# Kernel optimization log

Measured on AMD Instinct MI355X. Metric: run time of the kernel, lower is better.

The kernel has to match this reference:

```python
import jax, jax.numpy as jnp
import numpy as np

D = 1024      # EMBEDDING_DIM
H = 16        # ATTENTION_HEADS
HD = 64       # HEAD_DIM
B, S = 4, 2048
EPS = 1e-5


def setup_inputs() -> dict:
    key = jax.random.key(0)
    ks = jax.random.split(key, 16)
    std = 0.02
    inp = {
        "x": jax.random.normal(ks[0], (B, S, D), dtype=jnp.float32),
        # per-head Q/K/V weights stacked: [H, D, HD]
        "Wq": jax.random.normal(ks[1], (H, D, HD), dtype=jnp.float32) * std,
        "Wk": jax.random.normal(ks[2], (H, D, HD), dtype=jnp.float32) * std,
        "Wv": jax.random.normal(ks[3], (H, D, HD), dtype=jnp.float32) * std,
        "bq": jnp.zeros((H, HD), dtype=jnp.float32),
        "bk": jnp.zeros((H, HD), dtype=jnp.float32),
        "bv": jnp.zeros((H, HD), dtype=jnp.float32),
        "Wo": jax.random.normal(ks[4], (D, D), dtype=jnp.float32) * std,
        "bo": jnp.zeros((D,), dtype=jnp.float32),
        "W1": jax.random.normal(ks[5], (D, 4 * D), dtype=jnp.float32) * std,
        "b1": jnp.zeros((4 * D,), dtype=jnp.float32),
        "W2": jax.random.normal(ks[6], (4 * D, D), dtype=jnp.float32) * std,
        "b2": jnp.zeros((D,), dtype=jnp.float32),
        # single shared LayerNorm (same module used for both pre-norms)
        "gamma": jnp.ones((D,), dtype=jnp.float32),
        "beta": jnp.zeros((D,), dtype=jnp.float32),
    }
    return inp


def _layer_norm(x, gamma, beta):
    mu = jnp.mean(x, axis=-1, keepdims=True)
    var = jnp.mean(jnp.square(x - mu), axis=-1, keepdims=True)
    return (x - mu) * jax.lax.rsqrt(var + EPS) * gamma + beta


def _block(x, Wq, Wk, Wv, bq, bk, bv, Wo, bo, W1, b1, W2, b2, gamma, beta):
    # pre-norm attention
    h = _layer_norm(x, gamma, beta)                     # [B,S,D]
    Q = jnp.einsum('bsd,hdk->bhsk', h, Wq) + bq[None, :, None, :]
    K = jnp.einsum('bsd,hdk->bhsk', h, Wk) + bk[None, :, None, :]
    V = jnp.einsum('bsd,hdk->bhsk', h, Wv) + bv[None, :, None, :]
    scores = jnp.einsum('bhsk,bhtk->bhst', Q, K) / jnp.sqrt(jnp.float32(HD))
    causal = jnp.tril(jnp.ones((S, S), dtype=bool))     # True = keep
    scores = jnp.where(causal[None, None], scores, -jnp.inf)
    attn = jax.nn.softmax(scores, axis=-1)              # [B,H,S,S]
    out = jnp.einsum('bhst,bhtk->bhsk', attn, V)        # [B,H,S,HD]
    out = out.transpose(0, 2, 1, 3).reshape(x.shape[0], x.shape[1], D)
    x = x + out @ Wo + bo
    # pre-norm MLP (shared layer norm params)
    h2 = _layer_norm(x, gamma, beta)
    mlp = jax.nn.gelu(h2 @ W1 + b1, approximate=False) @ W2 + b2
    return x + mlp


def reference(x, Wq, Wk, Wv, bq, bk, bv, Wo, bo, W1, b1, W2, b2, gamma, beta):
    return _block(x, Wq, Wk, Wv, bq, bk, bv, Wo, bo, W1, b1, W2, b2, gamma, beta)
```

## Files before the change

kernel.cpp:

```cpp
#include <hip/hip_runtime.h>
#include <hip/hip_bf16.h>

typedef __bf16  bf16x8 __attribute__((ext_vector_type(8)));
typedef float   f32x4  __attribute__((ext_vector_type(4)));
typedef short   s16x8  __attribute__((ext_vector_type(8)));

typedef const __attribute__((address_space(1))) void g_void;
typedef __attribute__((address_space(3))) void l_void;

__device__ __forceinline__ short f2b(float x) {
    __hip_bfloat16 h = __float2bfloat16(x);
    return __builtin_bit_cast(short, h);
}

__device__ __forceinline__ int pk2(float lo, float hi) {
    return (int)(unsigned short)f2b(lo) | ((int)f2b(hi) << 16);
}

__device__ __forceinline__ float fast_gelu(float v) {
    const float a = fminf(2.3022082f * (v + 0.044715f * v * v * v), 126.0f);
    const float t = exp2f(a);
    return v * t / (t + 1.0f);
}

__device__ __forceinline__ f32x4 mfma16(s16x8 a, s16x8 b, f32x4 c) {
    return __builtin_amdgcn_mfma_f32_16x16x32_bf16(
        __builtin_bit_cast(bf16x8, a), __builtin_bit_cast(bf16x8, b), c, 0, 0, 0);
}

__global__ __launch_bounds__(256) void transpose_bf16(
    const float* __restrict__ src, short* __restrict__ dst, int R, int C) {
    __shared__ float tile[32][33];
    src += (size_t)blockIdx.z * R * C;
    dst += (size_t)blockIdx.z * R * C;
    const int c0 = blockIdx.x * 32, r0 = blockIdx.y * 32;
    const int tx = threadIdx.x & 31, ty = threadIdx.x >> 5;
#pragma unroll
    for (int i = 0; i < 32; i += 8)
        tile[ty + i][tx] = src[(size_t)(r0 + ty + i) * C + c0 + tx];
    __syncthreads();
#pragma unroll
    for (int i = 0; i < 32; i += 8)
        dst[(size_t)(c0 + ty + i) * R + r0 + tx] = f2b(tile[tx][ty + i]);
}

__global__ __launch_bounds__(256) void concat_bias(
    const float* __restrict__ bq, const float* __restrict__ bk,
    const float* __restrict__ bv, float* __restrict__ o) {
    int i = blockIdx.x * 256 + threadIdx.x;
    if (i < 1024)      o[i] = bq[i];
    else if (i < 2048) o[i] = bk[i - 1024];
    else if (i < 3072) o[i] = bv[i - 2048];
}

__global__ __launch_bounds__(256) void ln_bf16(
    const float* __restrict__ x, const float* __restrict__ gamma,
    const float* __restrict__ beta, short* __restrict__ out) {
    __shared__ float red[8];
    const int row = blockIdx.x, tid = threadIdx.x;
    const float4 v = *(const float4*)(x + (size_t)row * 1024 + tid * 4);
    float s = v.x + v.y + v.z + v.w;
    float q = v.x * v.x + v.y * v.y + v.z * v.z + v.w * v.w;
#pragma unroll
    for (int off = 32; off > 0; off >>= 1) {
        s += __shfl_xor(s, off);
        q += __shfl_xor(q, off);
    }
    if ((tid & 63) == 0) { red[(tid >> 6) * 2] = s; red[(tid >> 6) * 2 + 1] = q; }
    __syncthreads();
    s = red[0] + red[2] + red[4] + red[6];
    q = red[1] + red[3] + red[5] + red[7];
    const float mu = s * (1.0f / 1024.0f);
    const float var = q * (1.0f / 1024.0f) - mu * mu;
    const float rs = rsqrtf(var + 1e-5f);
    const float4 g  = *(const float4*)(gamma + tid * 4);
    const float4 bt = *(const float4*)(beta + tid * 4);
    short4 o;
    o.x = f2b((v.x - mu) * rs * g.x + bt.x);
    o.y = f2b((v.y - mu) * rs * g.y + bt.y);
    o.z = f2b((v.z - mu) * rs * g.z + bt.z);
    o.w = f2b((v.w - mu) * rs * g.w + bt.w);
    *(short4*)(out + (size_t)row * 1024 + tid * 4) = o;
}

template <int MODE, int SWZ>
__global__ __launch_bounds__(512) void gemm_bf16(
    const short* __restrict__ A, const short* __restrict__ Bt,
    const float* __restrict__ bias, const float* __restrict__ resid,
    float* __restrict__ outf, short* __restrict__ outb, short* __restrict__ vt,
    int M, int N, int K) {
    __shared__ __align__(16) short As[2 * 128 * 32];
    __shared__ __align__(16) short Bs[2 * 128 * 32];

    const int tid = threadIdx.x;
    const int wave = tid >> 6, lane = tid & 63;
    const int l16 = lane & 15, quad = lane >> 4;
    const int wm = wave & 3, wn = wave >> 2;
    const int gx = gridDim.x;
    const int g = blockIdx.y * gx + blockIdx.x;
    const int xcd = g & 7, s = g >> 3;
    int m0, n0;
    if (SWZ == 0) {
        const int nband = gx >> 3;
        const int sm = s / nband;
        const int sn = s - sm * nband;
        m0 = sm * 128;
        n0 = (xcd * nband + sn) * 128;
    } else {
        const int mband = gridDim.y >> 3;
        const int sm = s / gx;
        m0 = (xcd * mband + sm) * 128;
        n0 = (s - sm * gx) * 128;
    }
    const int lrow = lane >> 2;
    const int lcol = (lane & 3) * 8;

    f32x4 acc[2][4] = {};

    for (int kk = 0; kk < K; kk += 64) {
#pragma unroll
        for (int p = 0; p < 2; ++p) {
            const int r = wave * 16 + lrow;
            const short* ga = A + (size_t)(m0 + r) * K + kk + p * 32 + lcol;
            short* la = &As[p * 4096 + wave * 512];
            __builtin_amdgcn_global_load_lds((g_void*)ga, (l_void*)la, 16, 0, 0);
            const short* gb = Bt + (size_t)(n0 + r) * K + kk + p * 32 + lcol;
            short* lb = &Bs[p * 4096 + wave * 512];
            __builtin_amdgcn_global_load_lds((g_void*)gb, (l_void*)lb, 16, 0, 0);
        }
        __syncthreads();
#pragma unroll
        for (int p = 0; p < 2; ++p) {
            s16x8 a[2], b[4];
#pragma unroll
            for (int t = 0; t < 2; ++t)
                a[t] = *(const s16x8*)&As[p * 4096 + (wm * 32 + t * 16 + l16) * 32 + quad * 8];
#pragma unroll
            for (int t = 0; t < 4; ++t)
                b[t] = *(const s16x8*)&Bs[p * 4096 + (wn * 64 + t * 16 + l16) * 32 + quad * 8];
#pragma unroll
            for (int mt = 0; mt < 2; ++mt)
#pragma unroll
                for (int nt = 0; nt < 4; ++nt)
                    acc[mt][nt] = mfma16(a[mt], b[nt], acc[mt][nt]);
        }
        __syncthreads();
    }

#pragma unroll
    for (int mt = 0; mt < 2; ++mt) {
#pragma unroll
        for (int nt = 0; nt < 4; ++nt) {
            const int row = m0 + wm * 32 + mt * 16 + quad * 4;
            const int col = n0 + wn * 64 + nt * 16 + l16;
            const float bc = bias[col];
            float v[4];
#pragma unroll
            for (int r = 0; r < 4; ++r) v[r] = acc[mt][nt][r] + bc;

            if (MODE == 1) {
#pragma unroll
                for (int r = 0; r < 4; ++r) {
                    const size_t rr = (size_t)(row + r);
                    outf[rr * N + col] = v[r] + resid[rr * N + col];
                }
            } else {
#pragma unroll
                for (int r = 0; r < 4; ++r)
                    outb[(size_t)(row + r) * N + col] = f2b(fast_gelu(v[r]));
            }
        }
    }
}


#define MM(MH, NH, AF, BB)                                                   \
    _Pragma("unroll") for (int p = 0; p < 2; ++p)                            \
        _Pragma("unroll") for (int ii = 0; ii < 4; ++ii)                     \
            _Pragma("unroll") for (int jj = 0; jj < 2; ++jj)                 \
                acc[(MH) * 4 + ii][(NH) * 2 + jj] =                          \
                    mfma16(AF[ii][p], BB[jj][p],                             \
                           acc[(MH) * 4 + ii][(NH) * 2 + jj]);

#define PH_A                                                                 \
    __builtin_amdgcn_s_barrier();                                            \
    asm volatile("s_waitcnt lgkmcnt(0)" ::: "memory");                       \
    __builtin_amdgcn_sched_barrier(0);                                       \
    __builtin_amdgcn_s_setprio(1);

#define PH_B                                                                 \
    __builtin_amdgcn_s_setprio(0);                                           \
    __builtin_amdgcn_sched_barrier(0);

#define PH_C                                                                 \
    __builtin_amdgcn_sched_barrier(0);                                       \
    __builtin_amdgcn_s_barrier();                                            \
    __builtin_amdgcn_sched_barrier(0);

#define KTILE(BUF, S1, S2, S3, S4)                                           \
    {                                                                        \
        s16x8 af[4][2], bl[2][2], bh[2][2];                                  \
                                        \
        _Pragma("unroll") for (int ii = 0; ii < 4; ++ii)                     \
            _Pragma("unroll") for (int p = 0; p < 2; ++p)                    \
                af[ii][p] = LDA(BUF, ii, p);                                 \
        _Pragma("unroll") for (int jj = 0; jj < 2; ++jj)                     \
            _Pragma("unroll") for (int p = 0; p < 2; ++p)                    \
                bl[jj][p] = LDB(BUF, jj, p);                                 \
        asm volatile("s_waitcnt lgkmcnt(8)" ::: "memory");                   \
        PH_A;                                                                \
        MM(0, 0, af, bl);                                                    \
        PH_B;                                                                \
        S1;                                                                  \
        PH_C;                                                                \
                                         \
        _Pragma("unroll") for (int jj = 0; jj < 2; ++jj)                     \
            _Pragma("unroll") for (int p = 0; p < 2; ++p)                    \
                bh[jj][p] = LDB(BUF, 2 + jj, p);                             \
        PH_A;                                                                \
        MM(0, 1, af, bh);                                                    \
        PH_B;                                                                \
        S2;                                                                  \
        PH_C;                                                                \
                                         \
        _Pragma("unroll") for (int ii = 0; ii < 4; ++ii)                     \
            _Pragma("unroll") for (int p = 0; p < 2; ++p)                    \
                af[ii][p] = LDA(BUF, 4 + ii, p);                             \
        PH_A;                                                                \
        MM(1, 1, af, bh);                                                    \
        PH_B;                                                                \
        S3;                                                                  \
        PH_C;                                                                \
                          \
        PH_A;                                                                \
        MM(1, 0, af, bl);                                                    \
        PH_B;                                                                \
        S4;                                                                  \
        asm volatile("s_waitcnt vmcnt(6)" ::: "memory");                     \
        PH_C;                                                                \
    }

template <int MODE>
__global__ __launch_bounds__(512, 2) void gemm256(
    const short* __restrict__ A, const short* __restrict__ Bt,
    const float* __restrict__ bias, const float* __restrict__ resid,
    float* __restrict__ outf, short* __restrict__ outb, short* __restrict__ vt,
    int M, int N, int K) {
    __shared__ __align__(16) short As[32768];
    __shared__ __align__(16) short Bs[32768];

    const int tid = threadIdx.x;
    const int wave = tid >> 6, lane = tid & 63;
    const int l16 = lane & 15, quad = lane >> 4;
    const int wm = wave >> 2, wn = wave & 3;

    const int nwg = gridDim.x;
    const int g = blockIdx.x;
    const int wgid = (g & 7) * (nwg >> 3) + (g >> 3);
    const int mtiles = M >> 8;
    const int m0 = (wgid % mtiles) << 8;
    const int n0 = (wgid / mtiles) << 8;

    const int rc = l16 * 32 + ((quad * 8) ^ ((l16 >> 3) << 4));
    const int a_rd = wm * 8192 + rc;
    const int b_rd = (wn >> 1) * 8192 + (wn & 1) * 4096 + rc;

    auto LDA = [&](int buf, int i, int p) {
        return *(const s16x8*)&As[buf * 16384 + a_rd + (i * 2 + p) * 512];
    };
    auto LDB = [&](int buf, int j, int p) {
        return *(const s16x8*)&Bs[buf * 16384 + b_rd + (j * 2 + p) * 512];
    };

    int r0, c0, r1, c1;
    {
        int s = tid * 16;
        int lin = s ^ (((s >> 9) & 1) << 5);
        r0 = ((lin >> 11) << 4) + ((lin >> 6) & 15);
        c0 = (((lin >> 10) & 1) << 5) + ((lin & 63) >> 1);
        s = (tid + 512) * 16;
        lin = s ^ (((s >> 9) & 1) << 5);
        r1 = ((lin >> 11) << 4) + ((lin >> 6) & 15);
        c1 = (((lin >> 10) & 1) << 5) + ((lin & 63) >> 1);
    }

    const short* gA = A + (size_t)m0 * K;
    const short* gB = Bt + (size_t)n0 * K;

    auto STAGE = [&](const short* gbase, int half, int kk, short* lds) {
        const short* s0 = gbase + (size_t)(half * 128 + r0) * K + kk + c0;
        const short* s1 = gbase + (size_t)(half * 128 + r1) * K + kk + c1;
        short* d0 = lds + half * 8192 + wave * 512;
        short* d1 = lds + half * 8192 + 4096 + wave * 512;
        __builtin_amdgcn_global_load_lds((g_void*)s0, (l_void*)d0, 16, 0, 0);
        __builtin_amdgcn_global_load_lds((g_void*)s1, (l_void*)d1, 16, 0, 0);
    };

    f32x4 acc[8][4] = {};

    STAGE(gB, 0, 0, Bs);
    STAGE(gB, 1, 0, Bs);
    STAGE(gA, 0, 0, As);
    STAGE(gA, 1, 0, As);
    asm volatile("s_waitcnt vmcnt(4)" ::: "memory");
    STAGE(gB, 0, 64, Bs + 16384);
    STAGE(gB, 1, 64, Bs + 16384);
    STAGE(gA, 0, 64, As + 16384);
    asm volatile("s_waitcnt vmcnt(6)" ::: "memory");
    __builtin_amdgcn_s_barrier();
    __builtin_amdgcn_sched_barrier(0);

    const int NI = K >> 7;
    for (int it = 0; it < NI; ++it) {
        const int kT1 = (2 * it + 1) * 64;
        int kT2 = (2 * it + 2) * 64;
        if (kT2 > K - 64) kT2 = K - 64;
        int kT3 = (2 * it + 3) * 64;
        if (kT3 > K - 64) kT3 = K - 64;

        KTILE(0,
              STAGE(gA, 1, kT1, As + 16384),
              STAGE(gB, 0, kT2, Bs),
              STAGE(gB, 1, kT2, Bs),
              STAGE(gA, 0, kT2, As));
        KTILE(1,
              STAGE(gA, 1, kT2, As),
              STAGE(gB, 0, kT3, Bs + 16384),
              STAGE(gB, 1, kT3, Bs + 16384),
              STAGE(gA, 0, kT3, As + 16384));
    }
    asm volatile("s_waitcnt vmcnt(0)" ::: "memory");

#pragma unroll
    for (int i = 0; i < 8; ++i) {
#pragma unroll
        for (int j = 0; j < 4; ++j) {
            const int row = m0 + wm * 128 + i * 16 + quad * 4;
            const int col = n0 + wn * 64 + j * 16 + l16;
            const float bc = bias[col];
            float v[4];
#pragma unroll
            for (int r = 0; r < 4; ++r) v[r] = acc[i][j][r] + bc;

            if (MODE == 0) {
                const int sel = col >> 10, within = col & 1023;
                const int h = within >> 6, hd = within & 63;
                const size_t bidx = (size_t)row >> 11, sp = row & 2047;
                if (sel == 0) {
#pragma unroll
                    for (int r = 0; r < 4; ++r) v[r] *= 0.18033688011112042f;
                }
                if (sel < 2) {
#pragma unroll
                    for (int r = 0; r < 4; ++r)
                        outb[(size_t)sel * (8192ull * 1024) +
                             ((bidx * 16 + h) * 2048 + sp + r) * 64 + hd] = f2b(v[r]);
                } else {
                    short4 o4;
                    o4.x = f2b(v[0]); o4.y = f2b(v[1]);
                    o4.z = f2b(v[2]); o4.w = f2b(v[3]);
                    *(short4*)&vt[((bidx * 16 + h) * 64 + hd) * 2048 + sp] = o4;
                }
            } else if (MODE == 1) {
#pragma unroll
                for (int r = 0; r < 4; ++r) {
                    const size_t rr = (size_t)(row + r);
                    outf[rr * N + col] = v[r] + resid[rr * N + col];
                }
            } else {
#pragma unroll
                for (int r = 0; r < 4; ++r)
                    outb[(size_t)(row + r) * N + col] = f2b(fast_gelu(v[r]));
            }
        }
    }
}

#undef KTILE
#undef PH_A
#undef PH_B
#undef PH_C
#undef MM

__global__ __launch_bounds__(256) void attn_kernel(
    const short* __restrict__ Q, const short* __restrict__ K,
    const short* __restrict__ Vt, short* __restrict__ O) {
    const int bid = blockIdx.x;
    const int xcd = bid & 7;
    const int sub = (bid >> 3) & 7;
    const int grp = bid >> 6;
    const int bh  = grp * 8 + xcd;
    const int h = bh & 15, b = bh >> 4;
    const int gq = sub;
    const int tid = threadIdx.x, wave = tid >> 6, lane = tid & 63;
    const int l16 = lane & 15, quad = lane >> 4;

    __shared__ __align__(16) short Ks[2][64 * 72];
    __shared__ __align__(16) short Vts[2][64 * 72];
    __shared__ __align__(16) short Ps[4][16 * 72];

    const size_t bhoff = (size_t)bh * (2048ull * 64);
    const int srow = tid >> 2;
    const int sseg = (tid & 3) * 16;

    const int qts[4] = {gq, 15 - gq, 16 + gq, 31 - gq};

    for (int pass = 0; pass < 4; ++pass) {
        const int qt = qts[pass];
        const int q0 = qt * 64;
        const int q_lane = q0 + wave * 16 + l16;

        const short* qrow = Q + bhoff + (size_t)q_lane * 64;
        s16x8 bq0 = *(const s16x8*)(qrow + quad * 8);
        s16x8 bq1 = *(const s16x8*)(qrow + 32 + quad * 8);

        f32x4 oacc[4] = {};
        float lsum = 0.0f;

        s16x8 k0, k1, v0, v1;
        {
            const short* kg = K + bhoff + (size_t)srow * 64 + sseg;
            k0 = *(const s16x8*)kg;
            k1 = *(const s16x8*)(kg + 8);
            const short* vg = Vt + bhoff + (size_t)srow * 2048 + sseg;
            v0 = *(const s16x8*)vg;
            v1 = *(const s16x8*)(vg + 8);
        }

        for (int j = 0; j <= qt; ++j) {
            const int buf = j & 1;
            *(s16x8*)&Ks[buf][srow * 72 + sseg]      = k0;
            *(s16x8*)&Ks[buf][srow * 72 + sseg + 8]  = k1;
            *(s16x8*)&Vts[buf][srow * 72 + sseg]     = v0;
            *(s16x8*)&Vts[buf][srow * 72 + sseg + 8] = v1;
            __syncthreads();

            if (j < qt) {
                const short* kg = K + bhoff + (size_t)((j + 1) * 64 + srow) * 64 + sseg;
                k0 = *(const s16x8*)kg;
                k1 = *(const s16x8*)(kg + 8);
                const short* vg = Vt + bhoff + (size_t)srow * 2048 + (j + 1) * 64 + sseg;
                v0 = *(const s16x8*)vg;
                v1 = *(const s16x8*)(vg + 8);
            }

            f32x4 st[4];
#pragma unroll
            for (int s = 0; s < 4; ++s) {
                s16x8 ak0 = *(const s16x8*)&Ks[buf][(s * 16 + l16) * 72 + quad * 8];
                s16x8 ak1 = *(const s16x8*)&Ks[buf][(s * 16 + l16) * 72 + 32 + quad * 8];
                f32x4 c = {};
                c = mfma16(ak0, bq0, c);
                c = mfma16(ak1, bq1, c);
                st[s] = c;
            }
            if (j == qt) {
#pragma unroll
                for (int s = 0; s < 4; ++s)
#pragma unroll
                    for (int r = 0; r < 4; ++r) {
                        const int t = j * 64 + s * 16 + quad * 4 + r;
                        if (t > q_lane) st[s][r] = -3000.0f;
                    }
            }
            float rs = 0.0f;
#pragma unroll
            for (int s = 0; s < 4; ++s) {
#pragma unroll
                for (int r = 0; r < 4; ++r) {
                    st[s][r] = exp2f(st[s][r]);
                    rs += st[s][r];
                }
                int2 pw;
                pw.x = pk2(st[s][0], st[s][1]);
                pw.y = pk2(st[s][2], st[s][3]);
                *(int2*)&Ps[wave][l16 * 72 + s * 16 + quad * 4] = pw;
            }
            rs += __shfl_xor(rs, 16);
            rs += __shfl_xor(rs, 32);
            lsum += rs;

            asm volatile("s_waitcnt lgkmcnt(0)" ::: "memory");
            s16x8 ap0 = *(const s16x8*)&Ps[wave][l16 * 72 + quad * 8];
            s16x8 ap1 = *(const s16x8*)&Ps[wave][l16 * 72 + 32 + quad * 8];

#pragma unroll
            for (int nt = 0; nt < 4; ++nt) {
                s16x8 bv0 = *(const s16x8*)&Vts[buf][(nt * 16 + l16) * 72 + quad * 8];
                s16x8 bv1 = *(const s16x8*)&Vts[buf][(nt * 16 + l16) * 72 + 32 + quad * 8];
                oacc[nt] = mfma16(ap0, bv0, oacc[nt]);
                oacc[nt] = mfma16(ap1, bv1, oacc[nt]);
            }
        }
        __syncthreads();

        float inv[4];
#pragma unroll
        for (int r = 0; r < 4; ++r)
            inv[r] = 1.0f / __shfl(lsum, quad * 4 + r, 64);
#pragma unroll
        for (int nt = 0; nt < 4; ++nt)
#pragma unroll
            for (int r = 0; r < 4; ++r) {
                const int row = q0 + wave * 16 + quad * 4 + r;
                O[((size_t)b * 2048 + row) * 1024 + h * 64 + nt * 16 + l16] =
                    f2b(oacc[nt][r] * inv[r]);
            }
    }
}

extern "C" void kernel_launch(void* const* d_in, const int* in_sizes, int n_in,
                              void* d_out, int out_size, void* d_ws, size_t ws_size,
                              hipStream_t stream) {
    const float* x     = (const float*)d_in[0];
    const float* Wq    = (const float*)d_in[1];
    const float* Wk    = (const float*)d_in[2];
    const float* Wv    = (const float*)d_in[3];
    const float* bq    = (const float*)d_in[4];
    const float* bk    = (const float*)d_in[5];
    const float* bv    = (const float*)d_in[6];
    const float* Wo    = (const float*)d_in[7];
    const float* bo    = (const float*)d_in[8];
    const float* W1    = (const float*)d_in[9];
    const float* b1    = (const float*)d_in[10];
    const float* W2    = (const float*)d_in[11];
    const float* b2    = (const float*)d_in[12];
    const float* gamma = (const float*)d_in[13];
    const float* beta  = (const float*)d_in[14];
    float* out = (float*)d_out;

    char* ws = (char*)d_ws;
    size_t off = 0;
    auto alloc = [&](size_t bytes) -> char* {
        char* p = ws + off;
        off += (bytes + 255) & ~(size_t)255;
        return p;
    };
    short* h1    = (short*)alloc(8192ull * 1024 * 2);
    short* btqkv = (short*)alloc(3072ull * 1024 * 2);
    short* btwo  = (short*)alloc(1024ull * 1024 * 2);
    short* btw1  = (short*)alloc(4096ull * 1024 * 2);
    short* btw2  = (short*)alloc(1024ull * 4096 * 2);
    float* bqkv  = (float*)alloc(3072ull * 4);
    short* qkv   = (short*)alloc(2ull * 8192 * 1024 * 2);
    short* vt    = (short*)alloc(8192ull * 1024 * 2);
    short* aout  = (short*)alloc(8192ull * 1024 * 2);
    float* x2    = (float*)alloc(8192ull * 1024 * 4);
    short* h2    = (short*)alloc(8192ull * 1024 * 2);
    short* m1    = (short*)alloc(8192ull * 4096 * 2);

    transpose_bf16<<<dim3(2, 32, 16), 256, 0, stream>>>(Wq, btqkv, 1024, 64);
    transpose_bf16<<<dim3(2, 32, 16), 256, 0, stream>>>(Wk, btqkv + 1024ull * 1024, 1024, 64);
    transpose_bf16<<<dim3(2, 32, 16), 256, 0, stream>>>(Wv, btqkv + 2ull * 1024 * 1024, 1024, 64);
    transpose_bf16<<<dim3(32, 32, 1), 256, 0, stream>>>(Wo, btwo, 1024, 1024);
    transpose_bf16<<<dim3(128, 32, 1), 256, 0, stream>>>(W1, btw1, 1024, 4096);
    transpose_bf16<<<dim3(32, 128, 1), 256, 0, stream>>>(W2, btw2, 4096, 1024);
    concat_bias<<<12, 256, 0, stream>>>(bq, bk, bv, bqkv);

    ln_bf16<<<8192, 256, 0, stream>>>(x, gamma, beta, h1);
    gemm256<0><<<384, 512, 0, stream>>>(
        h1, btqkv, bqkv, nullptr, nullptr, qkv, vt, 8192, 3072, 1024);
    attn_kernel<<<512, 256, 0, stream>>>(
        qkv, qkv + 8192ull * 1024, vt, aout);
    gemm_bf16<1, 0><<<dim3(8, 64), 512, 0, stream>>>(
        aout, btwo, bo, x, x2, nullptr, nullptr, 8192, 1024, 1024);
    ln_bf16<<<8192, 256, 0, stream>>>(x2, gamma, beta, h2);
    gemm256<2><<<512, 512, 0, stream>>>(
        h2, btw1, b1, nullptr, nullptr, m1, nullptr, 8192, 4096, 1024);
    gemm_bf16<1, 1><<<dim3(8, 64), 512, 0, stream>>>(
        m1, btw2, b2, x2, out, nullptr, nullptr, 8192, 1024, 4096);
}
```

Before: 531.0 us.

## Reorder GEMM global-to-LDS prefetch stages and add QKV epilogue to small GEMM

The 256-tile GEMM's software pipeline is rescheduled. Each global_load_lds stage is now issued before its MFMA phase instead of after it, the prefetch order of A and B halves across K tiles is rotated, and the vmcnt waits in the prologue and loop are adjusted to match. The goal is to start memory traffic earlier and overlap it better with MFMA work. A MODE 0 (QKV scatter with Q pre-scaling and a V-transpose store) epilogue is also added to the smaller GEMM kernel, so that kernel can produce QKV output; this risks LDS hazards if the reordered waits are wrong.

Result: no change. 527.1 us (-0.7%).

```diff
diff --git a/kernel.cpp b/kernel.cpp
--- a/kernel.cpp
+++ b/kernel.cpp
@@ -158,7 +158,26 @@
 #pragma unroll
             for (int r = 0; r < 4; ++r) v[r] = acc[mt][nt][r] + bc;
 
-            if (MODE == 1) {
+            if (MODE == 0) {
+                const int sel = col >> 10, within = col & 1023;
+                const int h = within >> 6, hd = within & 63;
+                const size_t bidx = (size_t)row >> 11, sp = row & 2047;
+                if (sel == 0) {
+#pragma unroll
+                    for (int r = 0; r < 4; ++r) v[r] *= 0.18033688011112042f;
+                }
+                if (sel < 2) {
+#pragma unroll
+                    for (int r = 0; r < 4; ++r)
+                        outb[(size_t)sel * (8192ull * 1024) +
+                             ((bidx * 16 + h) * 2048 + sp + r) * 64 + hd] = f2b(v[r]);
+                } else {
+                    short4 o4;
+                    o4.x = f2b(v[0]); o4.y = f2b(v[1]);
+                    o4.z = f2b(v[2]); o4.w = f2b(v[3]);
+                    *(short4*)&vt[((bidx * 16 + h) * 64 + hd) * 2048 + sp] = o4;
+                }
+            } else if (MODE == 1) {
 #pragma unroll
                 for (int r = 0; r < 4; ++r) {
                     const size_t rr = (size_t)(row + r);
@@ -193,7 +212,6 @@
     __builtin_amdgcn_sched_barrier(0);
 
 #define PH_C                                                                 \
-    __builtin_amdgcn_sched_barrier(0);                                       \
     __builtin_amdgcn_s_barrier();                                            \
     __builtin_amdgcn_sched_barrier(0);
 
@@ -208,35 +226,35 @@
             _Pragma("unroll") for (int p = 0; p < 2; ++p)                    \
                 bl[jj][p] = LDB(BUF, jj, p);                                 \
         asm volatile("s_waitcnt lgkmcnt(8)" ::: "memory");                   \
+        S1;                                                                  \
         PH_A;                                                                \
         MM(0, 0, af, bl);                                                    \
         PH_B;                                                                \
-        S1;                                                                  \
         PH_C;                                                                \
                                          \
         _Pragma("unroll") for (int jj = 0; jj < 2; ++jj)                     \
             _Pragma("unroll") for (int p = 0; p < 2; ++p)                    \
                 bh[jj][p] = LDB(BUF, 2 + jj, p);                             \
+        S2;                                                                  \
         PH_A;                                                                \
         MM(0, 1, af, bh);                                                    \
         PH_B;                                                                \
-        S2;                                                                  \
         PH_C;                                                                \
                                          \
         _Pragma("unroll") for (int ii = 0; ii < 4; ++ii)                     \
             _Pragma("unroll") for (int p = 0; p < 2; ++p)                    \
                 af[ii][p] = LDA(BUF, 4 + ii, p);                             \
+        S3;                                                                  \
         PH_A;                                                                \
         MM(1, 1, af, bh);                                                    \
         PH_B;                                                                \
-        S3;                                                                  \
         PH_C;                                                                \
-                          \
+                       \
+        S4;                                                                  \
         PH_A;                                                                \
         MM(1, 0, af, bl);                                                    \
         PH_B;                                                                \
-        S4;                                                                  \
-        asm volatile("s_waitcnt vmcnt(6)" ::: "memory");                     \
+        asm volatile("s_waitcnt vmcnt(4)" ::: "memory");                     \
         PH_C;                                                                \
     }
 
@@ -302,11 +320,9 @@
     STAGE(gB, 1, 0, Bs);
     STAGE(gA, 0, 0, As);
     STAGE(gA, 1, 0, As);
-    asm volatile("s_waitcnt vmcnt(4)" ::: "memory");
     STAGE(gB, 0, 64, Bs + 16384);
     STAGE(gB, 1, 64, Bs + 16384);
-    STAGE(gA, 0, 64, As + 16384);
-    asm volatile("s_waitcnt vmcnt(6)" ::: "memory");
+    asm volatile("s_waitcnt vmcnt(4)" ::: "memory");
     __builtin_amdgcn_s_barrier();
     __builtin_amdgcn_sched_barrier(0);
 
@@ -319,15 +335,15 @@
         if (kT3 > K - 64) kT3 = K - 64;
 
         KTILE(0,
+              STAGE(gA, 0, kT1, As + 16384),
               STAGE(gA, 1, kT1, As + 16384),
               STAGE(gB, 0, kT2, Bs),
-              STAGE(gB, 1, kT2, Bs),
-              STAGE(gA, 0, kT2, As));
+              STAGE(gB, 1, kT2, Bs));
         KTILE(1,
+              STAGE(gA, 0, kT2, As),
               STAGE(gA, 1, kT2, As),
               STAGE(gB, 0, kT3, Bs + 16384),
-              STAGE(gB, 1, kT3, Bs + 16384),
-              STAGE(gA, 0, kT3, As + 16384));
+              STAGE(gB, 1, kT3, Bs + 16384));
     }
     asm volatile("s_waitcnt vmcnt(0)" ::: "memory");
 
```

## Hand-schedule GEMM LDS reads with inline asm and split lgkmcnt waits

Applied to the files above, without the earlier changes.

Replaces the compiler-generated LDS fragment loads in the 256x256 GEMM main loop with explicit ds_read_b128 inline asm at fixed offsets. The 32 MFMAs of each phase are split into two halves, each gated by a partial lgkmcnt wait, so matrix math can begin before every LDS read has returned. The global-to-LDS staging order is also changed: A tiles are prefetched earlier, the prologue issues fewer stages and the vmcnt thresholds are adjusted. The aim is to hide LDS latency and rebalance the prefetch pipeline. The hand-counted waitcnt values and the reordered buffer schedule risk races if any count is wrong.

New measurement: 523.1 us. About the same (-1.5%).

```diff
diff --git a/kernel.cpp b/kernel.cpp
--- a/kernel.cpp
+++ b/kernel.cpp
@@ -4,6 +4,7 @@
 typedef __bf16  bf16x8 __attribute__((ext_vector_type(8)));
 typedef float   f32x4  __attribute__((ext_vector_type(4)));
 typedef short   s16x8  __attribute__((ext_vector_type(8)));
+typedef int     i32x4  __attribute__((ext_vector_type(4)));
 
 typedef const __attribute__((address_space(1))) void g_void;
 typedef __attribute__((address_space(3))) void l_void;
@@ -27,6 +28,8 @@
     return __builtin_amdgcn_mfma_f32_16x16x32_bf16(
         __builtin_bit_cast(bf16x8, a), __builtin_bit_cast(bf16x8, b), c, 0, 0, 0);
 }
+
+#define S16(x) __builtin_bit_cast(s16x8, x)
 
 __global__ __launch_bounds__(256) void transpose_bf16(
     const float* __restrict__ src, short* __restrict__ dst, int R, int C) {
@@ -174,69 +177,72 @@
 }
 
 
-#define MM(MH, NH, AF, BB)                                                   \
-    _Pragma("unroll") for (int p = 0; p < 2; ++p)                            \
-        _Pragma("unroll") for (int ii = 0; ii < 4; ++ii)                     \
-            _Pragma("unroll") for (int jj = 0; jj < 2; ++jj)                 \
-                acc[(MH) * 4 + ii][(NH) * 2 + jj] =                          \
-                    mfma16(AF[ii][p], BB[jj][p],                             \
-                           acc[(MH) * 4 + ii][(NH) * 2 + jj]);
+#define DSR(dst, b, o)                                                       \
+    asm volatile("ds_read_b128 %0, %1 offset:" #o : "=v"(dst) : "v"(b))
+
+#define LGKM(n)                                                              \
+    asm volatile("s_waitcnt lgkmcnt(" #n ")" ::: "memory");                  \
+    __builtin_amdgcn_sched_barrier(0)
+
+#define MM8(MH, NH, A0, A1, A2, A3, B0, B1)                                  \
+    acc[(MH)*4+0][(NH)*2+0] = mfma16(S16(A0), S16(B0), acc[(MH)*4+0][(NH)*2+0]); \
+    acc[(MH)*4+0][(NH)*2+1] = mfma16(S16(A0), S16(B1), acc[(MH)*4+0][(NH)*2+1]); \
+    acc[(MH)*4+1][(NH)*2+0] = mfma16(S16(A1), S16(B0), acc[(MH)*4+1][(NH)*2+0]); \
+    acc[(MH)*4+1][(NH)*2+1] = mfma16(S16(A1), S16(B1), acc[(MH)*4+1][(NH)*2+1]); \
+    acc[(MH)*4+2][(NH)*2+0] = mfma16(S16(A2), S16(B0), acc[(MH)*4+2][(NH)*2+0]); \
+    acc[(MH)*4+2][(NH)*2+1] = mfma16(S16(A2), S16(B1), acc[(MH)*4+2][(NH)*2+1]); \
+    acc[(MH)*4+3][(NH)*2+0] = mfma16(S16(A3), S16(B0), acc[(MH)*4+3][(NH)*2+0]); \
+    acc[(MH)*4+3][(NH)*2+1] = mfma16(S16(A3), S16(B1), acc[(MH)*4+3][(NH)*2+1])
 
 #define PH_A                                                                 \
     __builtin_amdgcn_s_barrier();                                            \
-    asm volatile("s_waitcnt lgkmcnt(0)" ::: "memory");                       \
     __builtin_amdgcn_sched_barrier(0);                                       \
-    __builtin_amdgcn_s_setprio(1);
+    __builtin_amdgcn_s_setprio(1)
 
 #define PH_B                                                                 \
     __builtin_amdgcn_s_setprio(0);                                           \
-    __builtin_amdgcn_sched_barrier(0);
+    __builtin_amdgcn_sched_barrier(0)
 
 #define PH_C                                                                 \
-    __builtin_amdgcn_sched_barrier(0);                                       \
     __builtin_amdgcn_s_barrier();                                            \
-    __builtin_amdgcn_sched_barrier(0);
-
-#define KTILE(BUF, S1, S2, S3, S4)                                           \
+    __builtin_amdgcn_sched_barrier(0)
+
+#define KTILE(AR, BR, S1, S2, S3, S4)                                        \
     {                                                                        \
-        s16x8 af[4][2], bl[2][2], bh[2][2];                                  \
-                                        \
-        _Pragma("unroll") for (int ii = 0; ii < 4; ++ii)                     \
-            _Pragma("unroll") for (int p = 0; p < 2; ++p)                    \
-                af[ii][p] = LDA(BUF, ii, p);                                 \
-        _Pragma("unroll") for (int jj = 0; jj < 2; ++jj)                     \
-            _Pragma("unroll") for (int p = 0; p < 2; ++p)                    \
-                bl[jj][p] = LDB(BUF, jj, p);                                 \
-        asm volatile("s_waitcnt lgkmcnt(8)" ::: "memory");                   \
+        i32x4 a0,a1,a2,a3,a4,a5,a6,a7, b0,b1,b2,b3, h0,h1,h2,h3;             \
+         \
+        DSR(a0, AR, 0);    DSR(a1, AR, 2048); DSR(a2, AR, 4096); DSR(a3, AR, 6144); \
+        DSR(b0, BR, 0);    DSR(b1, BR, 2048);                                \
+        DSR(a4, AR, 1024); DSR(a5, AR, 3072); DSR(a6, AR, 5120); DSR(a7, AR, 7168); \
+        DSR(b2, BR, 1024); DSR(b3, BR, 3072);                                \
+        S1;                                                                  \
         PH_A;                                                                \
-        MM(0, 0, af, bl);                                                    \
+        LGKM(6); MM8(0, 0, a0, a1, a2, a3, b0, b1);                          \
+        LGKM(0); MM8(0, 0, a4, a5, a6, a7, b2, b3);                          \
+        PH_B; PH_C;                                                          \
+                                      \
+        DSR(h0, BR, 4096); DSR(h1, BR, 6144);                                \
+        DSR(h2, BR, 5120); DSR(h3, BR, 7168);                                \
+        S2;                                                                  \
+        PH_A;                                                                \
+        LGKM(2); MM8(0, 1, a0, a1, a2, a3, h0, h1);                          \
+        LGKM(0); MM8(0, 1, a4, a5, a6, a7, h2, h3);                          \
+        PH_B; PH_C;                                                          \
+                      \
+        DSR(a0, AR, 8192); DSR(a1, AR, 10240); DSR(a2, AR, 12288); DSR(a3, AR, 14336); \
+        DSR(a4, AR, 9216); DSR(a5, AR, 11264); DSR(a6, AR, 13312); DSR(a7, AR, 15360); \
+        S3;                                                                  \
+        PH_A;                                                                \
+        LGKM(4); MM8(1, 1, a0, a1, a2, a3, h0, h1);                          \
+        LGKM(0); MM8(1, 1, a4, a5, a6, a7, h2, h3);                          \
+        PH_B; PH_C;                                                          \
+                 \
+        S4;                                                                  \
+        PH_A;                                                                \
+        MM8(1, 0, a0, a1, a2, a3, b0, b1);                                   \
+        MM8(1, 0, a4, a5, a6, a7, b2, b3);                                   \
         PH_B;                                                                \
-        S1;                                                                  \
-        PH_C;                                                                \
-                                         \
-        _Pragma("unroll") for (int jj = 0; jj < 2; ++jj)                     \
-            _Pragma("unroll") for (int p = 0; p < 2; ++p)                    \
-                bh[jj][p] = LDB(BUF, 2 + jj, p);                             \
-        PH_A;                                                                \
-        MM(0, 1, af, bh);                                                    \
-        PH_B;                                                                \
-        S2;                                                                  \
-        PH_C;                                                                \
-                                         \
-        _Pragma("unroll") for (int ii = 0; ii < 4; ++ii)                     \
-            _Pragma("unroll") for (int p = 0; p < 2; ++p)                    \
-                af[ii][p] = LDA(BUF, 4 + ii, p);                             \
-        PH_A;                                                                \
-        MM(1, 1, af, bh);                                                    \
-        PH_B;                                                                \
-        S3;                                                                  \
-        PH_C;                                                                \
-                          \
-        PH_A;                                                                \
-        MM(1, 0, af, bl);                                                    \
-        PH_B;                                                                \
-        S4;                                                                  \
-        asm volatile("s_waitcnt vmcnt(6)" ::: "memory");                     \
+        asm volatile("s_waitcnt vmcnt(4)" ::: "memory");                     \
         PH_C;                                                                \
     }
 
@@ -265,12 +271,10 @@
     const int a_rd = wm * 8192 + rc;
     const int b_rd = (wn >> 1) * 8192 + (wn & 1) * 4096 + rc;
 
-    auto LDA = [&](int buf, int i, int p) {
-        return *(const s16x8*)&As[buf * 16384 + a_rd + (i * 2 + p) * 512];
-    };
-    auto LDB = [&](int buf, int j, int p) {
-        return *(const s16x8*)&Bs[buf * 16384 + b_rd + (j * 2 + p) * 512];
-    };
+    const uint32_t asb = (uint32_t)(uintptr_t)(l_void*)&As[0];
+    const uint32_t bsb = (uint32_t)(uintptr_t)(l_void*)&Bs[0];
+    const uint32_t aRd0 = asb + 2u * (uint32_t)a_rd, aRd1 = aRd0 + 32768u;
+    const uint32_t bRd0 = bsb + 2u * (uint32_t)b_rd, bRd1 = bRd0 + 32768u;
 
     int r0, c0, r1, c1;
     {
@@ -302,11 +306,9 @@
     STAGE(gB, 1, 0, Bs);
     STAGE(gA, 0, 0, As);
     STAGE(gA, 1, 0, As);
-    asm volatile("s_waitcnt vmcnt(4)" ::: "memory");
     STAGE(gB, 0, 64, Bs + 16384);
     STAGE(gB, 1, 64, Bs + 16384);
-    STAGE(gA, 0, 64, As + 16384);
-    asm volatile("s_waitcnt vmcnt(6)" ::: "memory");
+    asm volatile("s_waitcnt vmcnt(4)" ::: "memory");
     __builtin_amdgcn_s_barrier();
     __builtin_amdgcn_sched_barrier(0);
 
@@ -318,16 +320,16 @@
         int kT3 = (2 * it + 3) * 64;
         if (kT3 > K - 64) kT3 = K - 64;
 
-        KTILE(0,
+        KTILE(aRd0, bRd0,
+              STAGE(gA, 0, kT1, As + 16384),
               STAGE(gA, 1, kT1, As + 16384),
               STAGE(gB, 0, kT2, Bs),
-              STAGE(gB, 1, kT2, Bs),
-              STAGE(gA, 0, kT2, As));
-        KTILE(1,
+              STAGE(gB, 1, kT2, Bs));
+        KTILE(aRd1, bRd1,
+              STAGE(gA, 0, kT2, As),
               STAGE(gA, 1, kT2, As),
               STAGE(gB, 0, kT3, Bs + 16384),
-              STAGE(gB, 1, kT3, Bs + 16384),
-              STAGE(gA, 0, kT3, As + 16384));
+              STAGE(gB, 1, kT3, Bs + 16384));
     }
     asm volatile("s_waitcnt vmcnt(0)" ::: "memory");
 
@@ -380,7 +382,9 @@
 #undef PH_A
 #undef PH_B
 #undef PH_C
-#undef MM
+#undef MM8
+#undef LGKM
+#undef DSR
 
 __global__ __launch_bounds__(256) void attn_kernel(
     const short* __restrict__ Q, const short* __restrict__ K,
```
